# Kernel optimization log

Hardware: AMD Instinct MI355X
Metric: run time of the kernel (lower is better)

Reference implementation:

```python
import jax, jax.numpy as jnp
import numpy as np

IN_C, OUT_C = 32, 32
M1 = M2 = M3 = 12
CFT_M1 = CFT_M2 = M1 // 4  # 3
L_SEG, M_CHEB = 8, 6


def cft2d(x, m1, m2, L, M):
    # Piecewise Chebyshev projection along H (L segments, M polys), rFFT along W.
    # x: [N, C, H, W] -> complex [N, C, m1, m2]
    N, C, H, W = x.shape
    seg = H // L
    t = jnp.linspace(-1.0, 1.0, seg)
    theta = jnp.arccos(jnp.clip(t, -1.0, 1.0))
    P = jnp.cos(jnp.arange(M)[:, None] * theta[None, :])  # [M, seg] Chebyshev T_k
    xs = x.reshape(N, C, L, seg, W)
    coef = jnp.einsum('nclsw,ms->nclmw', xs, P) / seg      # [N,C,L,M,W]
    coef = coef.reshape(N, C, L * M, W)[:, :, :m1, :]      # keep first m1 coeffs
    return jnp.fft.rfft(coef, axis=-1)[:, :, :, :m2]       # [N,C,m1,m2] complex


def setup_inputs() -> dict:
    key = jax.random.key(0)
    ks = jax.random.split(key, 16)
    B, H, W, D = 4, 64, 64, 64
    scale = 1.0 / (IN_C * OUT_C)
    wshape = (IN_C, OUT_C, M1, M2, M3)
    inp = {'x': jax.random.normal(ks[0], (B, IN_C, H, W, D), dtype=jnp.float32)}
    for i in range(4):
        inp[f'w{i+1}_re'] = scale * jax.random.uniform(ks[1 + 2 * i], wshape, dtype=jnp.float32)
        inp[f'w{i+1}_im'] = scale * jax.random.uniform(ks[2 + 2 * i], wshape, dtype=jnp.float32)
    cft_flat = IN_C * CFT_M1 * CFT_M2 * 2  # 576
    hidden = (IN_C + OUT_C) * 2            # 128
    inp['mlp_w1'] = 0.02 * jax.random.normal(ks[9], (cft_flat, hidden), dtype=jnp.float32)
    inp['mlp_b1'] = jnp.zeros((hidden,), dtype=jnp.float32)
    inp['mlp_w2'] = 0.02 * jax.random.normal(ks[10], (hidden, OUT_C), dtype=jnp.float32)
    inp['mlp_b2'] = jnp.zeros((OUT_C,), dtype=jnp.float32)
    inp['corr_scale'] = jnp.float32(0.1)
    return inp


def reference(x, w1_re, w1_im, w2_re, w2_im, w3_re, w3_im, w4_re, w4_im,
              mlp_w1, mlp_b1, mlp_w2, mlp_b2, corr_scale):
    B, C, H, W, D = x.shape
    O = mlp_w2.shape[1]
    x_ft = jnp.fft.rfftn(x, axes=(-3, -2, -1))  # [B,C,H,W,D//2+1] complex64

    def mix(xb, wre, wim):
        return jnp.einsum('bixyz,ioxyz->boxyz', xb, wre + 1j * wim)

    out_ft = jnp.zeros((B, O, H, W, D // 2 + 1), dtype=x_ft.dtype)
    out_ft = out_ft.at[:, :, :M1, :M2, :M3].set(mix(x_ft[:, :, :M1, :M2, :M3], w1_re, w1_im))
    out_ft = out_ft.at[:, :, -M1:, :M2, :M3].set(mix(x_ft[:, :, -M1:, :M2, :M3], w2_re, w2_im))
    out_ft = out_ft.at[:, :, :M1, -M2:, :M3].set(mix(x_ft[:, :, :M1, -M2:, :M3], w3_re, w3_im))
    out_ft = out_ft.at[:, :, -M1:, -M2:, :M3].set(mix(x_ft[:, :, -M1:, -M2:, :M3], w4_re, w4_im))
    x_fno = jnp.fft.irfftn(out_ft, s=(H, W, D), axes=(-3, -2, -1))

    # Chebyshev-Fourier correction branch over depth slices
    xs = jnp.transpose(x, (0, 4, 1, 2, 3)).reshape(B * D, C, H, W)
    cft = cft2d(xs, CFT_M1, CFT_M2, L_SEG, M_CHEB)                 # [B*D,C,3,3] complex
    cft_flat = jnp.stack([cft.real, cft.imag], axis=-1).reshape(B * D, -1)  # view_as_real order
    h = jax.nn.gelu(cft_flat @ mlp_w1 + mlp_b1, approximate=False)
    corr = h @ mlp_w2 + mlp_b2                                     # [B*D, O]
    corr = jnp.transpose(corr.reshape(B, D, O), (0, 2, 1))[:, :, None, None, :]  # [B,O,1,1,D]
    return x_fno + corr_scale * corr
```

## Files before the change

### kernel.cpp

```cpp
#include <hip/hip_runtime.h>
#include <math.h>


static __device__ __forceinline__ void fill_tw(float2* tw, int tid, int nthr) {
    for (int m = tid; m < 64; m += nthr) {
        float s, c;
        sincosf((float)m * 0.09817477042468103f, &s, &c);
        tw[m] = make_float2(c, s);
    }
}

__global__ __launch_bounds__(256) void k_fwd_zy(const float* __restrict__ x,
                                                float2* __restrict__ X2) {
    __shared__ float xt[64 * 68];
    __shared__ float2 z1[64 * 12];
    __shared__ float2 tw[64];
    const int tid = threadIdx.x;
    const int blk = blockIdx.x;
    fill_tw(tw, tid, 256);
    const float4* xrow4 = (const float4*)(x + (size_t)blk * 4096);
    for (int r = 0; r < 4; ++r) {
        int i4 = r * 256 + tid;
        int w = i4 >> 4, d4 = (i4 & 15) << 2;
        float4 v = xrow4[i4];
        *(float4*)&xt[w * 68 + d4] = v;
    }
    __syncthreads();
    {
        const int w = tid >> 2, kz0 = (tid & 3) * 3;
        float2 a0 = make_float2(0.f, 0.f), a1 = a0, a2 = a0;
        const float* xr = &xt[w * 68];
        for (int d = 0; d < 64; ++d) {
            float xv = xr[d];
            float2 t0 = tw[(kz0 * d) & 63];
            float2 t1 = tw[((kz0 + 1) * d) & 63];
            float2 t2 = tw[((kz0 + 2) * d) & 63];
            a0.x += xv * t0.x; a0.y -= xv * t0.y;
            a1.x += xv * t1.x; a1.y -= xv * t1.y;
            a2.x += xv * t2.x; a2.y -= xv * t2.y;
        }
        z1[w * 12 + kz0]     = a0;
        z1[w * 12 + kz0 + 1] = a1;
        z1[w * 12 + kz0 + 2] = a2;
    }
    __syncthreads();
    float2* xout = X2 + (size_t)blk * 288;
    for (int idx = tid; idx < 288; idx += 256) {
        int a = idx / 12, kz = idx - a * 12;
        int kyv = a < 12 ? a : a + 40;
        float2 acc = make_float2(0.f, 0.f);
        for (int w = 0; w < 64; ++w) {
            float2 z = z1[w * 12 + kz];
            float2 t = tw[(kyv * w) & 63];
            acc.x += z.x * t.x + z.y * t.y;
            acc.y += z.y * t.x - z.x * t.y;
        }
        xout[idx] = acc;
    }
}

__global__ __launch_bounds__(256) void k_fwd_x(const float2* __restrict__ X2,
                                               float2* __restrict__ X3) {
    __shared__ float2 s2[64 * 12];
    __shared__ float2 tw[64];
    const int tid = threadIdx.x;
    const int blk = blockIdx.x;
    const int ay = blk % 24, bc = blk / 24;
    fill_tw(tw, tid, 256);
    const float2* src = X2 + (size_t)bc * (64 * 288) + ay * 12;
    for (int i = tid; i < 768; i += 256) {
        int hh = i / 12, kz = i - hh * 12;
        s2[i] = src[hh * 288 + kz];
    }
    __syncthreads();
    float2* dst = X3 + (size_t)bc * 6912 + ay * 12;
    for (int idx = tid; idx < 288; idx += 256) {
        int ax = idx / 12, kz = idx - ax * 12;
        int kxv = ax < 12 ? ax : ax + 40;
        float2 acc = make_float2(0.f, 0.f);
        for (int hh = 0; hh < 64; ++hh) {
            float2 z = s2[hh * 12 + kz];
            float2 t = tw[(kxv * hh) & 63];
            acc.x += z.x * t.x + z.y * t.y;
            acc.y += z.y * t.x - z.x * t.y;
        }
        dst[ax * 288 + kz] = acc;
    }
}

__global__ __launch_bounds__(384) void k_mix(const float2* __restrict__ X3,
                                             float2* __restrict__ F,
        const float* __restrict__ w1re, const float* __restrict__ w1im,
        const float* __restrict__ w2re, const float* __restrict__ w2im,
        const float* __restrict__ w3re, const float* __restrict__ w3im,
        const float* __restrict__ w4re, const float* __restrict__ w4im) {
    __shared__ float2 xs[128 * 12];
    const int tid = threadIdx.x;
    const int blk = blockIdx.x;
    const int ax = blk / 24, ay = blk % 24;
    const int cx = ax >= 12 ? 1 : 0, cy = ay >= 12 ? 1 : 0;
    const int m1 = ax - cx * 12, m2 = ay - cy * 12;
    const int sel = cx + cy * 2;
    const float* wre = sel == 0 ? w1re : sel == 1 ? w2re : sel == 2 ? w3re : w4re;
    const float* wim = sel == 0 ? w1im : sel == 1 ? w2im : sel == 2 ? w3im : w4im;
    const size_t moff = (size_t)ax * 288 + (size_t)ay * 12;
    for (int i = tid; i < 1536; i += 384) {
        int bi = i / 12, kz = i - bi * 12;
        xs[i] = X3[(size_t)bi * 6912 + moff + kz];
    }
    __syncthreads();
    const int o = tid / 12, kz = tid - (tid / 12) * 12;
    const int wbase = o * 1728 + m1 * 144 + m2 * 12 + kz;
    float2 A0 = make_float2(0.f, 0.f), A1 = A0, A2 = A0, A3 = A0;
    for (int i = 0; i < 32; ++i) {
        float wr = wre[i * 55296 + wbase];
        float wi = wim[i * 55296 + wbase];
        float2 x0 = xs[i * 12 + kz];
        float2 x1 = xs[(32 + i) * 12 + kz];
        float2 x2 = xs[(64 + i) * 12 + kz];
        float2 x3 = xs[(96 + i) * 12 + kz];
        A0.x += x0.x * wr - x0.y * wi; A0.y += x0.x * wi + x0.y * wr;
        A1.x += x1.x * wr - x1.y * wi; A1.y += x1.x * wi + x1.y * wr;
        A2.x += x2.x * wr - x2.y * wi; A2.y += x2.x * wi + x2.y * wr;
        A3.x += x3.x * wr - x3.y * wi; A3.y += x3.x * wi + x3.y * wr;
    }
    F[(size_t)(0 * 32 + o) * 6912 + moff + kz] = A0;
    F[(size_t)(1 * 32 + o) * 6912 + moff + kz] = A1;
    F[(size_t)(2 * 32 + o) * 6912 + moff + kz] = A2;
    F[(size_t)(3 * 32 + o) * 6912 + moff + kz] = A3;
}

__global__ __launch_bounds__(256) void k_inv_x(const float2* __restrict__ F,
                                               float2* __restrict__ Y1) {
    __shared__ float2 fs[24 * 12];
    __shared__ float2 tw[64];
    const int tid = threadIdx.x;
    const int blk = blockIdx.x;
    const int ay = blk % 24, bo = blk / 24;
    fill_tw(tw, tid, 256);
    const float2* src = F + (size_t)bo * 6912 + ay * 12;
    for (int i = tid; i < 288; i += 256) {
        int ax = i / 12, kz = i - ax * 12;
        fs[i] = src[ax * 288 + kz];
    }
    __syncthreads();
    float2* dst = Y1 + (size_t)bo * (64 * 288) + ay * 12;
    for (int idx = tid; idx < 768; idx += 256) {
        int hh = idx / 12, kz = idx - (idx / 12) * 12;
        float2 acc = make_float2(0.f, 0.f);
        for (int ax = 0; ax < 24; ++ax) {
            int kxv = ax < 12 ? ax : ax + 40;
            float2 f = fs[ax * 12 + kz];
            float2 t = tw[(kxv * hh) & 63];
            acc.x += f.x * t.x - f.y * t.y;
            acc.y += f.x * t.y + f.y * t.x;
        }
        dst[hh * 288 + kz] = acc;
    }
}

__global__ __launch_bounds__(256) void k_cft(const float* __restrict__ x,
                                             float* __restrict__ cft) {
    __shared__ float2 tw[64];
    __shared__ float red[3 * 64 * 18];
    const int tid = threadIdx.x;
    const int blk = blockIdx.x;
    const int d = tid & 63, q = tid >> 6;
    fill_tw(tw, tid, 256);
    __syncthreads();
    float aR[3][3] = {{0.f}}, aI[3][3] = {{0.f}};
    const float* xb = x + (size_t)blk * 262144;
    for (int wi = 0; wi < 16; ++wi) {
        const int w = q * 16 + wi;
        float c0 = 0.f, c1 = 0.f, c2 = 0.f;
        #pragma unroll
        for (int s = 0; s < 8; ++s) {
            float xv = xb[(size_t)(s * 64 + w) * 64 + d];
            float t = (2.0f * (float)s - 7.0f) * (1.0f / 7.0f);
            c0 += xv;
            c1 += xv * t;
            c2 += xv * (2.0f * t * t - 1.0f);
        }
        c0 *= 0.125f; c1 *= 0.125f; c2 *= 0.125f;
        #pragma unroll
        for (int f = 0; f < 3; ++f) {
            float2 t = tw[(f * w) & 63];
            aR[0][f] += c0 * t.x; aI[0][f] -= c0 * t.y;
            aR[1][f] += c1 * t.x; aI[1][f] -= c1 * t.y;
            aR[2][f] += c2 * t.x; aI[2][f] -= c2 * t.y;
        }
    }
    if (q > 0) {
        float* dst = &red[((q - 1) * 64 + d) * 18];
        #pragma unroll
        for (int k = 0; k < 3; ++k)
            #pragma unroll
            for (int f = 0; f < 3; ++f) {
                dst[k * 6 + f * 2]     = aR[k][f];
                dst[k * 6 + f * 2 + 1] = aI[k][f];
            }
    }
    __syncthreads();
    if (q == 0) {
        #pragma unroll
        for (int qq = 0; qq < 3; ++qq) {
            const float* sr = &red[(qq * 64 + d) * 18];
            #pragma unroll
            for (int k = 0; k < 3; ++k)
                #pragma unroll
                for (int f = 0; f < 3; ++f) {
                    aR[k][f] += sr[k * 6 + f * 2];
                    aI[k][f] += sr[k * 6 + f * 2 + 1];
                }
        }
        const int b = blk >> 5, c = blk & 31;
        float* dst = cft + (size_t)(b * 64 + d) * 576 + c * 18;
        #pragma unroll
        for (int k = 0; k < 3; ++k)
            #pragma unroll
            for (int f = 0; f < 3; ++f) {
                dst[k * 6 + f * 2]     = aR[k][f];
                dst[k * 6 + f * 2 + 1] = aI[k][f];
            }
    }
}

__global__ __launch_bounds__(128) void k_mlp(const float* __restrict__ cft,
                                             const float* __restrict__ w1,
                                             const float* __restrict__ b1,
                                             const float* __restrict__ w2,
                                             const float* __restrict__ b2,
                                             const float* __restrict__ cs,
                                             float* __restrict__ corr) {
    __shared__ float row[576];
    __shared__ float hbuf[128];
    const int n = blockIdx.x;
    const int tid = threadIdx.x;
    for (int i = tid; i < 576; i += 128) row[i] = cft[(size_t)n * 576 + i];
    __syncthreads();
    float acc = b1[tid];
    for (int k = 0; k < 576; ++k) acc += row[k] * w1[k * 128 + tid];
    hbuf[tid] = 0.5f * acc * (1.0f + erff(acc * 0.70710678118654752f));
    __syncthreads();
    if (tid < 32) {
        float a2 = b2[tid];
        for (int k = 0; k < 128; ++k) a2 += hbuf[k] * w2[k * 32 + tid];
        const int b = n >> 6, d = n & 63;
        corr[(b * 32 + tid) * 64 + d] = a2 * cs[0];
    }
}

__global__ __launch_bounds__(256) void k_inv_yz(const float2* __restrict__ Y1,
                                                const float* __restrict__ corr,
                                                float* __restrict__ out) {
    __shared__ float2 y1[288];
    __shared__ float2 y2[64 * 12];
    __shared__ float2 tw[64];
    __shared__ float corrl[64];
    const int tid = threadIdx.x;
    const int blk = blockIdx.x;
    const int bo = blk >> 6;
    fill_tw(tw, tid, 256);
    for (int i = tid; i < 288; i += 256) y1[i] = Y1[(size_t)blk * 288 + i];
    if (tid < 64) corrl[tid] = corr[bo * 64 + tid];
    __syncthreads();
    {
        const int w = tid >> 2, kz0 = (tid & 3) * 3;
        float2 a0 = make_float2(0.f, 0.f), a1 = a0, a2 = a0;
        for (int a = 0; a < 24; ++a) {
            int kyv = a < 12 ? a : a + 40;
            float2 t = tw[(kyv * w) & 63];
            float2 f0 = y1[a * 12 + kz0];
            float2 f1 = y1[a * 12 + kz0 + 1];
            float2 f2 = y1[a * 12 + kz0 + 2];
            a0.x += f0.x * t.x - f0.y * t.y; a0.y += f0.x * t.y + f0.y * t.x;
            a1.x += f1.x * t.x - f1.y * t.y; a1.y += f1.x * t.y + f1.y * t.x;
            a2.x += f2.x * t.x - f2.y * t.y; a2.y += f2.x * t.y + f2.y * t.x;
        }
        y2[w * 12 + kz0]     = a0;
        y2[w * 12 + kz0 + 1] = a1;
        y2[w * 12 + kz0 + 2] = a2;
    }
    float ctw[12], stw[12];
    const int d = tid & 63;
    #pragma unroll
    for (int kz = 0; kz < 12; ++kz) {
        float2 t = tw[(kz * d) & 63];
        float sc = (kz == 0 ? 1.0f : 2.0f) * (1.0f / 262144.0f);
        ctw[kz] = t.x * sc;
        stw[kz] = t.y * sc;
    }
    __syncthreads();
    const float cv = corrl[d];
    float* orow = out + (size_t)blk * 4096;
    const int wq = tid >> 6;
    for (int r = 0; r < 16; ++r) {
        int w = r * 4 + wq;
        float s = cv;
        #pragma unroll
        for (int kz = 0; kz < 12; ++kz) {
            float2 yv = y2[w * 12 + kz];
            s += yv.x * ctw[kz] - yv.y * stw[kz];
        }
        orow[w * 64 + d] = s;
    }
}

extern "C" void kernel_launch(void* const* d_in, const int* in_sizes, int n_in,
                              void* d_out, int out_size, void* d_ws, size_t ws_size,
                              hipStream_t stream) {
    const float* x    = (const float*)d_in[0];
    const float* w1re = (const float*)d_in[1];
    const float* w1im = (const float*)d_in[2];
    const float* w2re = (const float*)d_in[3];
    const float* w2im = (const float*)d_in[4];
    const float* w3re = (const float*)d_in[5];
    const float* w3im = (const float*)d_in[6];
    const float* w4re = (const float*)d_in[7];
    const float* w4im = (const float*)d_in[8];
    const float* mw1  = (const float*)d_in[9];
    const float* mb1  = (const float*)d_in[10];
    const float* mw2  = (const float*)d_in[11];
    const float* mb2  = (const float*)d_in[12];
    const float* cs   = (const float*)d_in[13];
    float* out = (float*)d_out;

    char* ws = (char*)d_ws;
    float2* X2   = (float2*)(ws);
    float2* X3   = (float2*)(ws + 18874368);
    float2* F    = (float2*)(ws + 25952256);
    float*  cft  = (float*) (ws + 33030144);
    float*  corr = (float*) (ws + 33619968);
    float2* Y1   = X2;

    hipLaunchKernelGGL(k_fwd_zy, dim3(8192), dim3(256), 0, stream, x, X2);
    hipLaunchKernelGGL(k_fwd_x,  dim3(3072), dim3(256), 0, stream, X2, X3);
    hipLaunchKernelGGL(k_mix,    dim3(576),  dim3(384), 0, stream, X3, F,
                       w1re, w1im, w2re, w2im, w3re, w3im, w4re, w4im);
    hipLaunchKernelGGL(k_inv_x,  dim3(3072), dim3(256), 0, stream, F, Y1);
    hipLaunchKernelGGL(k_cft,    dim3(128),  dim3(256), 0, stream, x, cft);
    hipLaunchKernelGGL(k_mlp,    dim3(256),  dim3(128), 0, stream,
                       cft, mw1, mb1, mw2, mb2, cs, corr);
    hipLaunchKernelGGL(k_inv_yz, dim3(8192), dim3(256), 0, stream, Y1, corr, out);
}
```

Before: 484.0 us.

## Exploit real-input symmetry in z DFT and precompute mode twiddle tables in shared memory

The forward z-direction DFT now folds the real input into even/odd pairs (x[d]±x[64-d]), halving the multiply count. All partial-DFT kernels precompute a per-mode twiddle table in shared memory, which removes the modular index arithmetic in the inner loops. Shared arrays are padded to reduce bank conflicts, and block sizes are changed to 384/288 so the work maps evenly onto threads. The cost is extra shared memory per block, which may lower occupancy, plus some extra syncs and table fills in every block.

```diff
diff --git a/kernel.cpp b/kernel.cpp
--- a/kernel.cpp
+++ b/kernel.cpp
@@ -2,90 +2,129 @@
 #include <math.h>
 
 
-static __device__ __forceinline__ void fill_tw(float2* tw, int tid, int nthr) {
+static __device__ __forceinline__ void fill_base(float2* twb, int tid, int nthr) {
     for (int m = tid; m < 64; m += nthr) {
         float s, c;
         sincosf((float)m * 0.09817477042468103f, &s, &c);
-        tw[m] = make_float2(c, s);
-    }
-}
-
-__global__ __launch_bounds__(256) void k_fwd_zy(const float* __restrict__ x,
+        twb[m] = make_float2(c, s);
+    }
+}
+
+static __device__ __forceinline__ void fill_mode(float2* twm, const float2* twb,
+                                                 int tid, int nthr) {
+    for (int i = tid; i < 24 * 64; i += nthr) {
+        int a = i >> 6, p = i & 63;
+        int kv = a < 12 ? a : a + 40;
+        twm[i] = twb[(kv * p) & 63];
+    }
+}
+
+__global__ __launch_bounds__(384) void k_fwd_zy(const float* __restrict__ x,
                                                 float2* __restrict__ X2) {
-    __shared__ float xt[64 * 68];
-    __shared__ float2 z1[64 * 12];
-    __shared__ float2 tw[64];
+    __shared__ union {
+        float  xt[64 * 68];
+        float2 uvb[32 * 64];
+    } U;
+    __shared__ float2 twz[32 * 12];
+    __shared__ float2 twm[24 * 64];
+    __shared__ float2 z1[64 * 14];
+    __shared__ float2 twb[64];
     const int tid = threadIdx.x;
     const int blk = blockIdx.x;
-    fill_tw(tw, tid, 256);
-    const float4* xrow4 = (const float4*)(x + (size_t)blk * 4096);
-    for (int r = 0; r < 4; ++r) {
-        int i4 = r * 256 + tid;
-        int w = i4 >> 4, d4 = (i4 & 15) << 2;
-        float4 v = xrow4[i4];
-        *(float4*)&xt[w * 68 + d4] = v;
-    }
-    __syncthreads();
+
+    const float4* xr4 = (const float4*)(x + (size_t)blk * 4096);
+    float4 ld[3]; int li[3]; int nld = 0;
+    for (int i4 = tid; i4 < 1024; i4 += 384) { li[nld] = i4; ld[nld] = xr4[i4]; ++nld; }
+    fill_base(twb, tid, 384);
+    for (int k = 0; k < nld; ++k) {
+        int i4 = li[k], w = i4 >> 4, d4 = (i4 & 15) << 2;
+        *(float4*)&U.xt[w * 68 + d4] = ld[k];
+    }
+    __syncthreads();
+
+    for (int i = tid; i < 32 * 12; i += 384) {
+        int d = i / 12, kz = i - d * 12;
+        twz[i] = twb[(kz * d) & 63];
+    }
+    fill_mode(twm, twb, tid, 384);
+
+    float2 uvv[6]; int ur[6], uw[6]; int nuv = 0;
+    for (int i = tid; i < 2048; i += 384) {
+        int d = i & 31, w = i >> 5;
+        float u, v; int r;
+        if (d == 0) { u = U.xt[w * 68]; v = U.xt[w * 68 + 32]; r = 31; }
+        else {
+            float a = U.xt[w * 68 + d], b = U.xt[w * 68 + 64 - d];
+            u = a + b; v = a - b; r = d - 1;
+        }
+        ur[nuv] = r; uw[nuv] = w; uvv[nuv] = make_float2(u, v); ++nuv;
+    }
+    __syncthreads();
+    for (int k = 0; k < nuv; ++k) U.uvb[ur[k] * 64 + uw[k]] = uvv[k];
+    __syncthreads();
+
     {
-        const int w = tid >> 2, kz0 = (tid & 3) * 3;
-        float2 a0 = make_float2(0.f, 0.f), a1 = a0, a2 = a0;
-        const float* xr = &xt[w * 68];
-        for (int d = 0; d < 64; ++d) {
-            float xv = xr[d];
-            float2 t0 = tw[(kz0 * d) & 63];
-            float2 t1 = tw[((kz0 + 1) * d) & 63];
-            float2 t2 = tw[((kz0 + 2) * d) & 63];
-            a0.x += xv * t0.x; a0.y -= xv * t0.y;
-            a1.x += xv * t1.x; a1.y -= xv * t1.y;
-            a2.x += xv * t2.x; a2.y -= xv * t2.y;
-        }
-        z1[w * 12 + kz0]     = a0;
-        z1[w * 12 + kz0 + 1] = a1;
-        z1[w * 12 + kz0 + 2] = a2;
-    }
-    __syncthreads();
-    float2* xout = X2 + (size_t)blk * 288;
-    for (int idx = tid; idx < 288; idx += 256) {
-        int a = idx / 12, kz = idx - a * 12;
-        int kyv = a < 12 ? a : a + 40;
+        const int w = tid & 63, q = tid >> 6;
+        float2 p = U.uvb[31 * 64 + w];
+        float re0 = p.x + p.y;
+        float re1 = p.x - p.y;
+        float im0 = 0.f, im1 = 0.f;
+        const float2* uvp = &U.uvb[w];
+        #pragma unroll
+        for (int d = 1; d <= 31; ++d) {
+            float2 uvd = uvp[(d - 1) * 64];
+            float4 t = *(const float4*)&twz[d * 12 + 2 * q];
+            re0 += uvd.x * t.x; im0 -= uvd.y * t.y;
+            re1 += uvd.x * t.z; im1 -= uvd.y * t.w;
+        }
+        *(float4*)&z1[w * 14 + 2 * q] = make_float4(re0, im0, re1, im1);
+    }
+    __syncthreads();
+
+    if (tid < 288) {
+        const int a = tid / 12, kz = tid - (tid / 12) * 12;
+        const float2* zp = &z1[kz];
+        const float2* tp = &twm[a * 64];
         float2 acc = make_float2(0.f, 0.f);
+        #pragma unroll
         for (int w = 0; w < 64; ++w) {
-            float2 z = z1[w * 12 + kz];
-            float2 t = tw[(kyv * w) & 63];
+            float2 z = zp[w * 14];
+            float2 t = tp[w];
             acc.x += z.x * t.x + z.y * t.y;
             acc.y += z.y * t.x - z.x * t.y;
         }
-        xout[idx] = acc;
-    }
-}
-
-__global__ __launch_bounds__(256) void k_fwd_x(const float2* __restrict__ X2,
+        X2[(size_t)blk * 288 + tid] = acc;
+    }
+}
+
+__global__ __launch_bounds__(288) void k_fwd_x(const float2* __restrict__ X2,
                                                float2* __restrict__ X3) {
-    __shared__ float2 s2[64 * 12];
-    __shared__ float2 tw[64];
-    const int tid = threadIdx.x;
-    const int blk = blockIdx.x;
-    const int ay = blk % 24, bc = blk / 24;
-    fill_tw(tw, tid, 256);
+    __shared__ float2 s2[64 * 14];
+    __shared__ float2 twm[24 * 64];
+    __shared__ float2 twb[64];
+    const int tid = threadIdx.x;
+    const int ay = blockIdx.x % 24, bc = blockIdx.x / 24;
     const float2* src = X2 + (size_t)bc * (64 * 288) + ay * 12;
-    for (int i = tid; i < 768; i += 256) {
-        int hh = i / 12, kz = i - hh * 12;
-        s2[i] = src[hh * 288 + kz];
-    }
-    __syncthreads();
-    float2* dst = X3 + (size_t)bc * 6912 + ay * 12;
-    for (int idx = tid; idx < 288; idx += 256) {
-        int ax = idx / 12, kz = idx - ax * 12;
-        int kxv = ax < 12 ? ax : ax + 40;
-        float2 acc = make_float2(0.f, 0.f);
-        for (int hh = 0; hh < 64; ++hh) {
-            float2 z = s2[hh * 12 + kz];
-            float2 t = tw[(kxv * hh) & 63];
-            acc.x += z.x * t.x + z.y * t.y;
-            acc.y += z.y * t.x - z.x * t.y;
-        }
-        dst[ax * 288 + kz] = acc;
-    }
+    for (int j = tid; j < 768; j += 288) {
+        int h = j / 12, kz = j - h * 12;
+        s2[h * 14 + kz] = src[h * 288 + kz];
+    }
+    fill_base(twb, tid, 288);
+    __syncthreads();
+    fill_mode(twm, twb, tid, 288);
+    __syncthreads();
+    const int ax = tid / 12, kz = tid - (tid / 12) * 12;
+    const float2* zp = &s2[kz];
+    const float2* tp = &twm[ax * 64];
+    float2 acc = make_float2(0.f, 0.f);
+    #pragma unroll
+    for (int h = 0; h < 64; ++h) {
+        float2 z = zp[h * 14];
+        float2 t = tp[h];
+        acc.x += z.x * t.x + z.y * t.y;
+        acc.y += z.y * t.x - z.x * t.y;
+    }
+    X3[(size_t)bc * 6912 + ax * 288 + ay * 12 + kz] = acc;
 }
 
 __global__ __launch_bounds__(384) void k_mix(const float2* __restrict__ X3,
@@ -130,28 +169,33 @@
     F[(size_t)(3 * 32 + o) * 6912 + moff + kz] = A3;
 }
 
-__global__ __launch_bounds__(256) void k_inv_x(const float2* __restrict__ F,
+__global__ __launch_bounds__(384) void k_inv_x(const float2* __restrict__ F,
                                                float2* __restrict__ Y1) {
-    __shared__ float2 fs[24 * 12];
-    __shared__ float2 tw[64];
-    const int tid = threadIdx.x;
-    const int blk = blockIdx.x;
-    const int ay = blk % 24, bo = blk / 24;
-    fill_tw(tw, tid, 256);
+    __shared__ float2 fs[24 * 14];
+    __shared__ float2 twm[24 * 64];
+    __shared__ float2 twb[64];
+    const int tid = threadIdx.x;
+    const int ay = blockIdx.x % 24, bo = blockIdx.x / 24;
     const float2* src = F + (size_t)bo * 6912 + ay * 12;
-    for (int i = tid; i < 288; i += 256) {
-        int ax = i / 12, kz = i - ax * 12;
-        fs[i] = src[ax * 288 + kz];
-    }
+    for (int j = tid; j < 288; j += 384) {
+        int ax = j / 12, kz = j - ax * 12;
+        fs[ax * 14 + kz] = src[ax * 288 + kz];
+    }
+    fill_base(twb, tid, 384);
+    __syncthreads();
+    fill_mode(twm, twb, tid, 384);
     __syncthreads();
     float2* dst = Y1 + (size_t)bo * (64 * 288) + ay * 12;
-    for (int idx = tid; idx < 768; idx += 256) {
+    #pragma unroll
+    for (int r = 0; r < 2; ++r) {
+        int idx = r * 384 + tid;
         int hh = idx / 12, kz = idx - (idx / 12) * 12;
+        const float2* fp = &fs[kz];
         float2 acc = make_float2(0.f, 0.f);
+        #pragma unroll
         for (int ax = 0; ax < 24; ++ax) {
-            int kxv = ax < 12 ? ax : ax + 40;
-            float2 f = fs[ax * 12 + kz];
-            float2 t = tw[(kxv * hh) & 63];
+            float2 f = fp[ax * 14];
+            float2 t = twm[ax * 64 + hh];
             acc.x += f.x * t.x - f.y * t.y;
             acc.y += f.x * t.y + f.y * t.x;
         }
@@ -166,7 +210,7 @@
     const int tid = threadIdx.x;
     const int blk = blockIdx.x;
     const int d = tid & 63, q = tid >> 6;
-    fill_tw(tw, tid, 256);
+    fill_base(tw, tid, 256);
     __syncthreads();
     float aR[3][3] = {{0.f}}, aI[3][3] = {{0.f}};
     const float* xb = x + (size_t)blk * 262144;
@@ -250,59 +294,64 @@
     }
 }
 
-__global__ __launch_bounds__(256) void k_inv_yz(const float2* __restrict__ Y1,
+__global__ __launch_bounds__(384) void k_inv_yz(const float2* __restrict__ Y1,
                                                 const float* __restrict__ corr,
                                                 float* __restrict__ out) {
-    __shared__ float2 y1[288];
-    __shared__ float2 y2[64 * 12];
-    __shared__ float2 tw[64];
+    __shared__ float2 y1s[24 * 16];
+    __shared__ float2 y2[64 * 14];
+    __shared__ float2 twm[24 * 64];
+    __shared__ float2 twb[64];
     __shared__ float corrl[64];
     const int tid = threadIdx.x;
     const int blk = blockIdx.x;
     const int bo = blk >> 6;
-    fill_tw(tw, tid, 256);
-    for (int i = tid; i < 288; i += 256) y1[i] = Y1[(size_t)blk * 288 + i];
+    for (int j = tid; j < 288; j += 384) {
+        int a = j / 12, kz = j - a * 12;
+        y1s[a * 16 + kz] = Y1[(size_t)blk * 288 + j];
+    }
     if (tid < 64) corrl[tid] = corr[bo * 64 + tid];
+    fill_base(twb, tid, 384);
+    __syncthreads();
+    fill_mode(twm, twb, tid, 384);
     __syncthreads();
     {
-        const int w = tid >> 2, kz0 = (tid & 3) * 3;
-        float2 a0 = make_float2(0.f, 0.f), a1 = a0, a2 = a0;
+        const int w = tid & 63, q = tid >> 6;
+        float a0x = 0.f, a0y = 0.f, a1x = 0.f, a1y = 0.f;
+        #pragma unroll
         for (int a = 0; a < 24; ++a) {
-            int kyv = a < 12 ? a : a + 40;
-            float2 t = tw[(kyv * w) & 63];
-            float2 f0 = y1[a * 12 + kz0];
-            float2 f1 = y1[a * 12 + kz0 + 1];
-            float2 f2 = y1[a * 12 + kz0 + 2];
-            a0.x += f0.x * t.x - f0.y * t.y; a0.y += f0.x * t.y + f0.y * t.x;
-            a1.x += f1.x * t.x - f1.y * t.y; a1.y += f1.x * t.y + f1.y * t.x;
-            a2.x += f2.x * t.x - f2.y * t.y; a2.y += f2.x * t.y + f2.y * t.x;
-        }
-        y2[w * 12 + kz0]     = a0;
-        y2[w * 12 + kz0 + 1] = a1;
-        y2[w * 12 + kz0 + 2] = a2;
-    }
-    float ctw[12], stw[12];
-    const int d = tid & 63;
+            float4 f = *(const float4*)&y1s[a * 16 + 2 * q];
+            float2 t = twm[a * 64 + w];
+            a0x += f.x * t.x - f.y * t.y;  a0y += f.x * t.y + f.y * t.x;
+            a1x += f.z * t.x - f.w * t.y;  a1y += f.z * t.y + f.w * t.x;
+        }
+        *(float4*)&y2[w * 14 + 2 * q] = make_float4(a0x, a0y, a1x, a1y);
+    }
+    const int d = tid & 63, wg = tid >> 6;
+    float ct[12], st[12];
     #pragma unroll
     for (int kz = 0; kz < 12; ++kz) {
-        float2 t = tw[(kz * d) & 63];
+        float2 t = twb[(kz * d) & 63];
         float sc = (kz == 0 ? 1.0f : 2.0f) * (1.0f / 262144.0f);
-        ctw[kz] = t.x * sc;
-        stw[kz] = t.y * sc;
-    }
-    __syncthreads();
+        ct[kz] = t.x * sc;
+        st[kz] = t.y * sc;
+    }
     const float cv = corrl[d];
+    __syncthreads();
     float* orow = out + (size_t)blk * 4096;
-    const int wq = tid >> 6;
-    for (int r = 0; r < 16; ++r) {
-        int w = r * 4 + wq;
-        float s = cv;
-        #pragma unroll
-        for (int kz = 0; kz < 12; ++kz) {
-            float2 yv = y2[w * 12 + kz];
-            s += yv.x * ctw[kz] - yv.y * stw[kz];
-        }
-        orow[w * 64 + d] = s;
+    #pragma unroll
+    for (int j = 0; j < 11; ++j) {
+        int w = wg + 6 * j;
+        if (w < 64) {
+            const float4* yp = (const float4*)&y2[w * 14];
+            float s = cv;
+            #pragma unroll
+            for (int kk = 0; kk < 6; ++kk) {
+                float4 yv = yp[kk];
+                s += yv.x * ct[2 * kk]     - yv.y * st[2 * kk];
+                s += yv.z * ct[2 * kk + 1] - yv.w * st[2 * kk + 1];
+            }
+            orow[w * 64 + d] = s;
+        }
     }
 }
 
@@ -333,13 +382,13 @@
     float*  corr = (float*) (ws + 33619968);
     float2* Y1   = X2;
 
-    hipLaunchKernelGGL(k_fwd_zy, dim3(8192), dim3(256), 0, stream, x, X2);
-    hipLaunchKernelGGL(k_fwd_x,  dim3(3072), dim3(256), 0, stream, X2, X3);
+    hipLaunchKernelGGL(k_fwd_zy, dim3(8192), dim3(384), 0, stream, x, X2);
+    hipLaunchKernelGGL(k_fwd_x,  dim3(3072), dim3(288), 0, stream, X2, X3);
     hipLaunchKernelGGL(k_mix,    dim3(576),  dim3(384), 0, stream, X3, F,
                        w1re, w1im, w2re, w2im, w3re, w3im, w4re, w4im);
-    hipLaunchKernelGGL(k_inv_x,  dim3(3072), dim3(256), 0, stream, F, Y1);
+    hipLaunchKernelGGL(k_inv_x,  dim3(3072), dim3(384), 0, stream, F, Y1);
     hipLaunchKernelGGL(k_cft,    dim3(128),  dim3(256), 0, stream, x, cft);
     hipLaunchKernelGGL(k_mlp,    dim3(256),  dim3(128), 0, stream,
                        cft, mw1, mb1, mw2, mb2, cs, corr);
-    hipLaunchKernelGGL(k_inv_yz, dim3(8192), dim3(256), 0, stream, Y1, corr, out);
-}
+    hipLaunchKernelGGL(k_inv_yz, dim3(8192), dim3(384), 0, stream, Y1, corr, out);
+}
```

New measurement: 570.7 us. 1.18x slower.
